# Kernel optimization log

Measured on AMD Instinct MI355X. Metric: run time of the kernel, lower is better.

Reference implementation:

```python
import jax, jax.numpy as jnp
import numpy as np

B, C, H, W = 2, 128, 192, 192
K = 9  # 3x3 kernel points
EPS = 1e-5


def conv3x3(x, w, b):
    # plain conv, stride 1, zero pad 1 (the pack's conv_offset_mask)
    out = jax.lax.conv_general_dilated(x, w, (1, 1), ((1, 1), (1, 1)),
                                       dimension_numbers=('NCHW', 'OIHW', 'NCHW'))
    return out + b[None, :, None, None]


def bilinear_gather(img, py, px):
    # img: (C,H,W); py/px: (K,H,W) float sampling coords; zero outside (DCNv2 semantics)
    y0 = jnp.floor(py)
    x0 = jnp.floor(px)
    ay = py - y0
    ax = px - x0
    y0i = y0.astype(jnp.int32)
    x0i = x0.astype(jnp.int32)

    def corner(yi, xi, wgt):
        valid = (yi >= 0) & (yi <= H - 1) & (xi >= 0) & (xi <= W - 1)
        yc = jnp.clip(yi, 0, H - 1)
        xc = jnp.clip(xi, 0, W - 1)
        v = img[:, yc, xc]  # (C,K,H,W) gather
        return v * (wgt * valid)[None]

    return (corner(y0i, x0i, (1 - ay) * (1 - ax))
            + corner(y0i, x0i + 1, (1 - ay) * ax)
            + corner(y0i + 1, x0i, ay * (1 - ax))
            + corner(y0i + 1, x0i + 1, ay * ax))


def dcn(x, lo, w_om, b_om, w, b):
    # ModulatedDeformConvPack: offsets+mask predicted from lo, deform conv applied to x
    om = conv3x3(lo, w_om, b_om)                      # (B, 3K, H, W)
    o1, o2, m = jnp.split(om, 3, axis=1)
    offset = jnp.concatenate([o1, o2], axis=1)        # (B, 2K, H, W)
    offset = offset.reshape(B, K, 2, H, W)            # channel 2k=y, 2k+1=x
    dy, dx = offset[:, :, 0], offset[:, :, 1]         # (B,K,H,W)
    mask = jax.nn.sigmoid(m)                          # (B,K,H,W)
    ky = jnp.array([-1, -1, -1, 0, 0, 0, 1, 1, 1], jnp.float32)
    kx = jnp.array([-1, 0, 1, -1, 0, 1, -1, 0, 1], jnp.float32)
    ii = jnp.arange(H, dtype=jnp.float32)[None, :, None]
    jj = jnp.arange(W, dtype=jnp.float32)[None, None, :]
    py = ii + ky[:, None, None] + dy                  # (B,K,H,W)
    px = jj + kx[:, None, None] + dx
    sampled = jax.vmap(bilinear_gather)(x, py, px)    # (B,C,K,H,W)
    sampled = sampled * mask[:, None]                 # modulation
    out = jnp.einsum('bckhw,ock->bohw', sampled, w.reshape(C, C, K))
    return out + b[None, :, None, None]


def inorm(x):
    # InstanceNorm2d(affine=False), eps=1e-5
    mu = x.mean((2, 3), keepdims=True)
    var = x.var((2, 3), keepdims=True)
    return (x - mu) * jax.lax.rsqrt(var + EPS)


def setup_inputs() -> dict:
    key = jax.random.key(0)
    ks = jax.random.split(key, 10)
    x = jax.random.normal(ks[0], (B, C, H, W), jnp.float32)
    lo = jax.random.normal(ks[1], (B, C, H, W), jnp.float32)
    # offset/mask conv kept small so sampling offsets stay near the grid
    w_om1 = jax.random.normal(ks[2], (3 * K, C, 3, 3), jnp.float32) * 0.01
    b_om1 = jnp.zeros((3 * K,), jnp.float32)
    w1 = jax.random.normal(ks[3], (C, C, 3, 3), jnp.float32) * 0.05
    b1 = jax.random.normal(ks[4], (C,), jnp.float32) * 0.02
    w_om2 = jax.random.normal(ks[5], (3 * K, C, 3, 3), jnp.float32) * 0.01
    b_om2 = jnp.zeros((3 * K,), jnp.float32)
    w2 = jax.random.normal(ks[6], (C, C, 3, 3), jnp.float32) * 0.05
    b2 = jax.random.normal(ks[7], (C,), jnp.float32) * 0.02
    return {'x': x, 'lo': lo, 'w_om1': w_om1, 'b_om1': b_om1, 'w1': w1, 'b1': b1,
            'w_om2': w_om2, 'b_om2': b_om2, 'w2': w2, 'b2': b2}


def reference(x, lo, w_om1, b_om1, w1, b1, w_om2, b_om2, w2, b2):
    r = jax.nn.relu(inorm(dcn(x, lo, w_om1, b_om1, w1, b1)))
    r = inorm(dcn(r, lo, w_om2, b_om2, w2, b2))
    return x + r
```

## Files before the change

### kernel.cpp

```cpp
#include <hip/hip_runtime.h>
#include <hip/hip_bf16.h>
#include <math.h>

#define BB 2
#define CCH 128
#define HH 192
#define WW 192
#define KK 9
#define HWs (HH*WW)
#define NPIX (BB*HWs)

typedef short bf16x8 __attribute__((ext_vector_type(8)));
typedef float f32x4 __attribute__((ext_vector_type(4)));

__device__ __forceinline__ int iclamp(int v, int lo, int hi) {
    return v < lo ? lo : (v > hi ? hi : v);
}
__device__ __forceinline__ unsigned short f2bf(float f) {
    union { __hip_bfloat16 h; unsigned short u; } cvt;
    cvt.h = __float2bfloat16(f);
    return cvt.u;
}
__device__ __forceinline__ float bflo(unsigned u) {
    return __uint_as_float(u << 16);
}
__device__ __forceinline__ float bfhi(unsigned u) {
    return __uint_as_float(u & 0xFFFF0000u);
}
__device__ __forceinline__ unsigned pkbf(float lo, float hi) {
    return (unsigned)f2bf(lo) | ((unsigned)f2bf(hi) << 16);
}

__global__ void transpose_wb_kernel(const float* __restrict__ in,
                                    unsigned short* __restrict__ outp) {
    int idx = blockIdx.x * 256 + threadIdx.x;
    if (idx >= 9 * CCH * CCH) return;
    int c = idx % CCH;
    int o = (idx / CCH) % CCH;
    int tap = idx / (CCH * CCH);
    outp[idx] = f2bf(in[(o * CCH + c) * 9 + tap]);
}

__global__ void transpose_womb_kernel(const float* __restrict__ in,
                                      unsigned short* __restrict__ outp) {
    int idx = blockIdx.x * 256 + threadIdx.x;
    if (idx >= 9 * 32 * CCH) return;
    int c = idx % CCH;
    int o = (idx / CCH) % 32;
    int tap = idx / (CCH * 32);
    outp[idx] = (o < 27) ? f2bf(in[(o * CCH + c) * 9 + tap]) : 0;
}

__global__ __launch_bounds__(256) void to_nhwc_bf16(
    const float* __restrict__ in, unsigned short* __restrict__ outp,
    const float* __restrict__ mu, const float* __restrict__ rs, int do_relu) {
    __shared__ float tile[CCH][33];
    int blk = blockIdx.x;
    int xt = blk % 6;
    int y = (blk / 6) % HH;
    int b = blk / (6 * HH);
    int x0 = xt * 32;
    int t = threadIdx.x;
    int xr = (t & 7) * 4;
    int cr = t >> 3;
#pragma unroll
    for (int it = 0; it < 4; ++it) {
        int c = it * 32 + cr;
        float4 v = *(const float4*)&in[((size_t)(b * CCH + c) * HH + y) * WW + x0 + xr];
        if (mu != nullptr) {
            float m = mu[b * CCH + c], r = rs[b * CCH + c];
            v.x = (v.x - m) * r; v.y = (v.y - m) * r;
            v.z = (v.z - m) * r; v.w = (v.w - m) * r;
        }
        if (do_relu) {
            v.x = fmaxf(v.x, 0.f); v.y = fmaxf(v.y, 0.f);
            v.z = fmaxf(v.z, 0.f); v.w = fmaxf(v.w, 0.f);
        }
        tile[c][xr] = v.x; tile[c][xr + 1] = v.y;
        tile[c][xr + 2] = v.z; tile[c][xr + 3] = v.w;
    }
    __syncthreads();
    int px = t >> 3;
    int wp = t & 7;
    size_t wbase = (((size_t)(b * HH + y)) * WW + x0 + px) * (CCH / 2);
    unsigned* outw = (unsigned*)outp;
#pragma unroll
    for (int it = 0; it < 8; ++it) {
        int ch = it * 16 + wp * 2;
        outw[wbase + it * 8 + wp] = pkbf(tile[ch][px], tile[ch + 1][px]);
    }
}

__global__ __launch_bounds__(256) void om_mfma_kernel(
    const unsigned short* __restrict__ lob,
    const unsigned short* __restrict__ Wob,
    const float* __restrict__ bom,
    float* __restrict__ samp) {
    __shared__ float s_om[4][16 * 33];
    int bid = blockIdx.x;
    int blk = (bid & 7) * 144 + (bid >> 3);
    int xt = blk % 3;
    int y = (blk / 3) % HH;
    int b = blk / (3 * HH);
    int t = threadIdx.x;
    int l = t & 63, q = l & 15, g = l >> 4, w = t >> 6;
    int px = xt * 64 + w * 16 + q;
    int cb = g * 8;
    f32x4 acc0 = (f32x4)0.f, acc1 = (f32x4)0.f;

    for (int k = 0; k < KK; ++k) {
        int ty = k / 3 - 1, tx = k % 3 - 1;
        int yy = y + ty, xx = px + tx;
        bool ok = (yy >= 0 && yy < HH && xx >= 0 && xx < WW);
        int yyc = iclamp(yy, 0, HH - 1), xxc = iclamp(xx, 0, WW - 1);
        const unsigned short* lrow = lob + ((size_t)(b * HH + yyc) * WW + xxc) * CCH;
#pragma unroll
        for (int ch = 0; ch < 4; ++ch) {
            bf16x8 a0 = *(const bf16x8*)&Wob[((size_t)k * 32 + q) * CCH + ch * 32 + cb];
            bf16x8 a1 = *(const bf16x8*)&Wob[((size_t)k * 32 + 16 + q) * CCH + ch * 32 + cb];
            bf16x8 bb = *(const bf16x8*)&lrow[ch * 32 + cb];
            if (!ok) bb = (bf16x8)0;
            acc0 = __builtin_amdgcn_mfma_f32_16x16x32_bf16(a0, bb, acc0, 0, 0, 0);
            acc1 = __builtin_amdgcn_mfma_f32_16x16x32_bf16(a1, bb, acc1, 0, 0, 0);
        }
    }
    float* so = s_om[w];
#pragma unroll
    for (int r = 0; r < 4; ++r) {
        int o0 = g * 4 + r;
        so[q * 33 + o0] = acc0[r] + bom[o0];
        int o1 = 16 + g * 4 + r;
        so[q * 33 + o1] = acc1[r] + ((o1 < 27) ? bom[o1] : 0.f);
    }
    __syncthreads();

    for (int tt = g; tt < 9; tt += 4) {
        float dy = so[q * 33 + 2 * tt];
        float dx = so[q * 33 + 2 * tt + 1];
        float ml = so[q * 33 + 18 + tt];
        float m = 1.0f / (1.0f + __expf(-ml));
        float py = (float)y + (float)(tt / 3 - 1) + dy;
        float pxf = (float)px + (float)(tt % 3 - 1) + dx;
        py = fminf(fmaxf(py, -2.0f), (float)(HH + 1));
        pxf = fminf(fmaxf(pxf, -2.0f), (float)(WW + 1));
        float y0f = floorf(py), x0f = floorf(pxf);
        float ay = py - y0f, ax = pxf - x0f;
        int y0 = (int)y0f, x0i = (int)x0f;
        int y1 = y0 + 1, x1 = x0i + 1;
        bool vy0 = (y0 >= 0 && y0 < HH), vy1 = (y1 >= 0 && y1 < HH);
        bool vx0 = (x0i >= 0 && x0i < WW), vx1 = (x1 >= 0 && x1 < WW);
        int y0c = iclamp(y0, 0, HH - 1), y1c = iclamp(y1, 0, HH - 1);
        int x0c = iclamp(x0i, 0, WW - 1), x1c = iclamp(x1, 0, WW - 1);
        float w00 = (1.0f - ay) * (1.0f - ax) * ((vy0 && vx0) ? m : 0.0f);
        float w01 = (1.0f - ay) * ax * ((vy0 && vx1) ? m : 0.0f);
        float w10 = ay * (1.0f - ax) * ((vy1 && vx0) ? m : 0.0f);
        float w11 = ay * ax * ((vy1 && vx1) ? m : 0.0f);
        float4 s0, s1;
        s0.x = __int_as_float(y0c * WW + x0c);
        s0.y = __int_as_float(y0c * WW + x1c);
        s0.z = __int_as_float(y1c * WW + x0c);
        s0.w = __int_as_float(y1c * WW + x1c);
        s1.x = w00; s1.y = w01; s1.z = w10; s1.w = w11;
        float* sp = samp + (((size_t)blk * 9 + tt) * 64 + w * 16 + q) * 8;
        *(float4*)sp = s0;
        *(float4*)(sp + 4) = s1;
    }
}

__global__ __launch_bounds__(256) void dcn_kernel(
    const unsigned short* __restrict__ xb,
    const float* __restrict__ samp,
    const unsigned short* __restrict__ Wb,
    const float* __restrict__ bias,
    float* __restrict__ outp) {
    __shared__ unsigned short s_w[CCH * CCH];
    int bid = blockIdx.x;
    int blk = (bid & 7) * 144 + (bid >> 3);
    int xt = blk % 3;
    int y = (blk / 3) % HH;
    int b = blk / (3 * HH);
    int t = threadIdx.x;
    int l = t & 63, q = l & 15, g = l >> 4, w = t >> 6;
    int px = xt * 64 + w * 16 + q;
    int cb = g * 8;
    int p_in = w * 16 + q;
    const unsigned short* xbb = xb + (size_t)b * HWs * CCH;
    const float* rec = samp + (size_t)blk * 9 * 64 * 8;
    char* swb = (char*)s_w;
    int swz_t = ((t >> 4) & 7) << 4;
    int xorq = (q & 7) << 4;

    f32x4 acc[8];
#pragma unroll
    for (int ot = 0; ot < 8; ++ot) acc[ot] = (f32x4)0.f;

    float4 rA = *(const float4*)(rec + (size_t)p_in * 8);
    float4 rB = *(const float4*)(rec + (size_t)p_in * 8 + 4);
    for (int k = 0; k < KK; ++k) {
        const char* wk = (const char*)(Wb + (size_t)k * CCH * CCH);
#pragma unroll
        for (int j = 0; j < 8; ++j) {
            int off = j * 4096 + t * 16;
            uint4 v = *(const uint4*)(wk + off);
            *(uint4*)(swb + (off ^ swz_t)) = v;
        }
        int kn = (k < 8) ? k + 1 : 8;
        float4 nA = *(const float4*)(rec + ((size_t)kn * 64 + p_in) * 8);
        float4 nB = *(const float4*)(rec + ((size_t)kn * 64 + p_in) * 8 + 4);
        int i00 = __float_as_int(rA.x);
        int i01 = __float_as_int(rA.y);
        int i10 = __float_as_int(rA.z);
        int i11 = __float_as_int(rA.w);
        const unsigned short* p00 = xbb + (size_t)i00 * CCH + cb;
        const unsigned short* p01 = xbb + (size_t)i01 * CCH + cb;
        const unsigned short* p10 = xbb + (size_t)i10 * CCH + cb;
        const unsigned short* p11 = xbb + (size_t)i11 * CCH + cb;
        bf16x8 bbv[4];
#pragma unroll
        for (int ch = 0; ch < 4; ++ch) {
            uint4 c00 = *(const uint4*)(p00 + ch * 32);
            uint4 c01 = *(const uint4*)(p01 + ch * 32);
            uint4 c10 = *(const uint4*)(p10 + ch * 32);
            uint4 c11 = *(const uint4*)(p11 + ch * 32);
            unsigned bbw[4];
            const unsigned* u00 = (const unsigned*)&c00;
            const unsigned* u01 = (const unsigned*)&c01;
            const unsigned* u10 = (const unsigned*)&c10;
            const unsigned* u11 = (const unsigned*)&c11;
#pragma unroll
            for (int d = 0; d < 4; ++d) {
                float slo = rB.x * bflo(u00[d]) + rB.y * bflo(u01[d]) +
                            rB.z * bflo(u10[d]) + rB.w * bflo(u11[d]);
                float shi = rB.x * bfhi(u00[d]) + rB.y * bfhi(u01[d]) +
                            rB.z * bfhi(u10[d]) + rB.w * bfhi(u11[d]);
                bbw[d] = pkbf(slo, shi);
            }
            uint4 bbu = make_uint4(bbw[0], bbw[1], bbw[2], bbw[3]);
            bbv[ch] = __builtin_bit_cast(bf16x8, bbu);
        }
        __syncthreads();
#pragma unroll
        for (int ch = 0; ch < 4; ++ch) {
            int inner = (ch * 64 + g * 16) ^ xorq;
#pragma unroll
            for (int ot = 0; ot < 8; ++ot) {
                bf16x8 a = *(const bf16x8*)(swb + (ot * 4096 + q * 256 + inner));
                acc[ot] = __builtin_amdgcn_mfma_f32_16x16x32_bf16(a, bbv[ch], acc[ot], 0, 0, 0);
            }
        }
        __syncthreads();
        rA = nA; rB = nB;
    }
#pragma unroll
    for (int ot = 0; ot < 8; ++ot) {
#pragma unroll
        for (int r = 0; r < 4; ++r) {
            int o = ot * 16 + g * 4 + r;
            outp[((size_t)(b * CCH + o) * HH + y) * WW + px] = acc[ot][r] + bias[o];
        }
    }
}

__global__ __launch_bounds__(256) void stats_kernel(
    const float* __restrict__ d, float* __restrict__ mu,
    float* __restrict__ rs) {
    int ch = blockIdx.x;
    const float* p = d + (size_t)ch * HWs;
    float s = 0.0f, s2 = 0.0f;
    for (int i = threadIdx.x; i < HWs / 4; i += 256) {
        float4 v = *(const float4*)&p[(size_t)i * 4];
        s += v.x + v.y + v.z + v.w;
        s2 += v.x * v.x + v.y * v.y + v.z * v.z + v.w * v.w;
    }
#pragma unroll
    for (int off = 32; off > 0; off >>= 1) {
        s += __shfl_down(s, off);
        s2 += __shfl_down(s2, off);
    }
    __shared__ float red[8];
    int wid = threadIdx.x >> 6;
    if ((threadIdx.x & 63) == 0) { red[wid] = s; red[4 + wid] = s2; }
    __syncthreads();
    if (threadIdx.x == 0) {
        s = red[0] + red[1] + red[2] + red[3];
        s2 = red[4] + red[5] + red[6] + red[7];
        float m = s / (float)HWs;
        float var = s2 / (float)HWs - m * m;
        mu[ch] = m;
        rs[ch] = rsqrtf(var + 1e-5f);
    }
}

__global__ __launch_bounds__(256) void final_kernel(
    const float* __restrict__ x, float* __restrict__ outp,
    const float* __restrict__ mu, const float* __restrict__ rs) {
    size_t i = ((size_t)blockIdx.x * 256 + threadIdx.x) * 4;
    int ch = (int)(i / HWs);
    float4 xv = *(const float4*)&x[i];
    float4 dv = *(const float4*)&outp[i];
    float m = mu[ch], r = rs[ch];
    float4 ov;
    ov.x = xv.x + (dv.x - m) * r;
    ov.y = xv.y + (dv.y - m) * r;
    ov.z = xv.z + (dv.z - m) * r;
    ov.w = xv.w + (dv.w - m) * r;
    *(float4*)&outp[i] = ov;
}

extern "C" void kernel_launch(void* const* d_in, const int* in_sizes, int n_in,
                              void* d_out, int out_size, void* d_ws,
                              size_t ws_size, hipStream_t stream) {
    (void)in_sizes; (void)n_in; (void)out_size; (void)ws_size;
    const float* x    = (const float*)d_in[0];
    const float* lo   = (const float*)d_in[1];
    const float* wom1 = (const float*)d_in[2];
    const float* bom1 = (const float*)d_in[3];
    const float* w1   = (const float*)d_in[4];
    const float* b1   = (const float*)d_in[5];
    const float* wom2 = (const float*)d_in[6];
    const float* bom2 = (const float*)d_in[7];
    const float* w2   = (const float*)d_in[8];
    const float* b2   = (const float*)d_in[9];
    float* out = (float*)d_out;

    char* wsb = (char*)d_ws;
    unsigned short* xbf  = (unsigned short*)wsb;
    unsigned short* lobf = (unsigned short*)(wsb + 18874368);
    float* samp = (float*)(wsb + 2 * 18874368);
    char* wp = wsb + 2 * 18874368 + 21233664;
    unsigned short* Wb1   = (unsigned short*)wp;
    unsigned short* Wb2   = (unsigned short*)(wp + 294912);
    unsigned short* Womb1 = (unsigned short*)(wp + 2 * 294912);
    unsigned short* Womb2 = (unsigned short*)(wp + 2 * 294912 + 73728);
    float* mu1 = (float*)(wp + 2 * 294912 + 2 * 73728);
    float* rs1 = mu1 + 256;
    float* mu2 = rs1 + 256;
    float* rs2 = mu2 + 256;

    transpose_wb_kernel<<<576, 256, 0, stream>>>(w1, Wb1);
    transpose_wb_kernel<<<576, 256, 0, stream>>>(w2, Wb2);
    transpose_womb_kernel<<<144, 256, 0, stream>>>(wom1, Womb1);
    transpose_womb_kernel<<<144, 256, 0, stream>>>(wom2, Womb2);

    to_nhwc_bf16<<<2304, 256, 0, stream>>>(x, xbf, nullptr, nullptr, 0);
    to_nhwc_bf16<<<2304, 256, 0, stream>>>(lo, lobf, nullptr, nullptr, 0);

    om_mfma_kernel<<<1152, 256, 0, stream>>>(lobf, Womb1, bom1, samp);
    dcn_kernel<<<1152, 256, 0, stream>>>(xbf, samp, Wb1, b1, out);
    stats_kernel<<<256, 256, 0, stream>>>(out, mu1, rs1);
    to_nhwc_bf16<<<2304, 256, 0, stream>>>(out, xbf, mu1, rs1, 1);

    om_mfma_kernel<<<1152, 256, 0, stream>>>(lobf, Womb2, bom2, samp);
    dcn_kernel<<<1152, 256, 0, stream>>>(xbf, samp, Wb2, b2, out);
    stats_kernel<<<256, 256, 0, stream>>>(out, mu2, rs2);

    final_kernel<<<9216, 256, 0, stream>>>(x, out, mu2, rs2);
}
```

Measured before the change: 450.9 us.

## Pre-gather all taps then double-buffer pre-swizzled weights in LDS

The DCN kernel now gathers and bilinearly interpolates the sampled inputs for all nine taps up front into registers (36 bf16x8 vectors per thread). It then runs the MFMA loop over a double-buffered LDS weight tile, prefetching the next tap's weights from global memory while the current tap computes, so there is one barrier per tap instead of two. The weight transpose kernel now writes the LDS swizzle into global memory, which removes the XOR from the staging stores. This raises register pressure considerably and doubles LDS use to 64KB per block, which could lower occupancy or cause spills.

```diff
diff --git a/kernel.cpp b/kernel.cpp
--- a/kernel.cpp
+++ b/kernel.cpp
@@ -31,14 +31,15 @@
     return (unsigned)f2bf(lo) | ((unsigned)f2bf(hi) << 16);
 }
 
-__global__ void transpose_wb_kernel(const float* __restrict__ in,
-                                    unsigned short* __restrict__ outp) {
+__global__ void transpose_wsw_kernel(const float* __restrict__ in,
+                                     unsigned short* __restrict__ outp) {
     int idx = blockIdx.x * 256 + threadIdx.x;
     if (idx >= 9 * CCH * CCH) return;
-    int c = idx % CCH;
-    int o = (idx / CCH) % CCH;
+    int col = idx % CCH;
+    int row = (idx / CCH) % CCH;
     int tap = idx / (CCH * CCH);
-    outp[idx] = f2bf(in[(o * CCH + c) * 9 + tap]);
+    int c = col ^ ((row & 7) << 3);
+    outp[idx] = f2bf(in[(row * CCH + c) * 9 + tap]);
 }
 
 __global__ void transpose_womb_kernel(const float* __restrict__ in,
@@ -170,10 +171,10 @@
 __global__ __launch_bounds__(256) void dcn_kernel(
     const unsigned short* __restrict__ xb,
     const float* __restrict__ samp,
-    const unsigned short* __restrict__ Wb,
+    const unsigned short* __restrict__ Wsw,
     const float* __restrict__ bias,
     float* __restrict__ outp) {
-    __shared__ unsigned short s_w[CCH * CCH];
+    __shared__ unsigned short s_w[2][CCH * CCH];
     int bid = blockIdx.x;
     int blk = (bid & 7) * 144 + (bid >> 3);
     int xt = blk % 3;
@@ -186,27 +187,13 @@
     int p_in = w * 16 + q;
     const unsigned short* xbb = xb + (size_t)b * HWs * CCH;
     const float* rec = samp + (size_t)blk * 9 * 64 * 8;
-    char* swb = (char*)s_w;
-    int swz_t = ((t >> 4) & 7) << 4;
     int xorq = (q & 7) << 4;
 
-    f32x4 acc[8];
-#pragma unroll
-    for (int ot = 0; ot < 8; ++ot) acc[ot] = (f32x4)0.f;
-
-    float4 rA = *(const float4*)(rec + (size_t)p_in * 8);
-    float4 rB = *(const float4*)(rec + (size_t)p_in * 8 + 4);
-    for (int k = 0; k < KK; ++k) {
-        const char* wk = (const char*)(Wb + (size_t)k * CCH * CCH);
-#pragma unroll
-        for (int j = 0; j < 8; ++j) {
-            int off = j * 4096 + t * 16;
-            uint4 v = *(const uint4*)(wk + off);
-            *(uint4*)(swb + (off ^ swz_t)) = v;
-        }
-        int kn = (k < 8) ? k + 1 : 8;
-        float4 nA = *(const float4*)(rec + ((size_t)kn * 64 + p_in) * 8);
-        float4 nB = *(const float4*)(rec + ((size_t)kn * 64 + p_in) * 8 + 4);
+    bf16x8 bbv[9][4];
+#pragma unroll
+    for (int k = 0; k < 9; ++k) {
+        float4 rA = *(const float4*)(rec + ((size_t)k * 64 + p_in) * 8);
+        float4 rB = *(const float4*)(rec + ((size_t)k * 64 + p_in) * 8 + 4);
         int i00 = __float_as_int(rA.x);
         int i01 = __float_as_int(rA.y);
         int i10 = __float_as_int(rA.z);
@@ -215,7 +202,6 @@
         const unsigned short* p01 = xbb + (size_t)i01 * CCH + cb;
         const unsigned short* p10 = xbb + (size_t)i10 * CCH + cb;
         const unsigned short* p11 = xbb + (size_t)i11 * CCH + cb;
-        bf16x8 bbv[4];
 #pragma unroll
         for (int ch = 0; ch < 4; ++ch) {
             uint4 c00 = *(const uint4*)(p00 + ch * 32);
@@ -236,21 +222,54 @@
                 bbw[d] = pkbf(slo, shi);
             }
             uint4 bbu = make_uint4(bbw[0], bbw[1], bbw[2], bbw[3]);
-            bbv[ch] = __builtin_bit_cast(bf16x8, bbu);
-        }
-        __syncthreads();
+            bbv[k][ch] = __builtin_bit_cast(bf16x8, bbu);
+        }
+    }
+
+    const char* wg = (const char*)Wsw;
+    {
+        uint4 st[8];
+#pragma unroll
+        for (int j = 0; j < 8; ++j)
+            st[j] = *(const uint4*)(wg + j * 4096 + t * 16);
+#pragma unroll
+        for (int j = 0; j < 8; ++j)
+            *(uint4*)((char*)s_w[0] + j * 4096 + t * 16) = st[j];
+    }
+    __syncthreads();
+
+    f32x4 acc[8];
+#pragma unroll
+    for (int ot = 0; ot < 8; ++ot) acc[ot] = (f32x4)0.f;
+
+#pragma unroll
+    for (int k = 0; k < 9; ++k) {
+        uint4 nx[8];
+        if (k < 8) {
+            const char* wn = wg + (size_t)(k + 1) * 32768;
+#pragma unroll
+            for (int j = 0; j < 8; ++j)
+                nx[j] = *(const uint4*)(wn + j * 4096 + t * 16);
+        }
+        char* swb = (char*)s_w[k & 1];
 #pragma unroll
         for (int ch = 0; ch < 4; ++ch) {
             int inner = (ch * 64 + g * 16) ^ xorq;
 #pragma unroll
             for (int ot = 0; ot < 8; ++ot) {
                 bf16x8 a = *(const bf16x8*)(swb + (ot * 4096 + q * 256 + inner));
-                acc[ot] = __builtin_amdgcn_mfma_f32_16x16x32_bf16(a, bbv[ch], acc[ot], 0, 0, 0);
+                acc[ot] = __builtin_amdgcn_mfma_f32_16x16x32_bf16(a, bbv[k][ch], acc[ot], 0, 0, 0);
             }
         }
+        if (k < 8) {
+            char* swn = (char*)s_w[(k + 1) & 1];
+#pragma unroll
+            for (int j = 0; j < 8; ++j)
+                *(uint4*)(swn + j * 4096 + t * 16) = nx[j];
+        }
         __syncthreads();
-        rA = nA; rB = nB;
-    }
+    }
+
 #pragma unroll
     for (int ot = 0; ot < 8; ++ot) {
 #pragma unroll
@@ -337,8 +356,8 @@
     float* mu2 = rs1 + 256;
     float* rs2 = mu2 + 256;
 
-    transpose_wb_kernel<<<576, 256, 0, stream>>>(w1, Wb1);
-    transpose_wb_kernel<<<576, 256, 0, stream>>>(w2, Wb2);
+    transpose_wsw_kernel<<<576, 256, 0, stream>>>(w1, Wb1);
+    transpose_wsw_kernel<<<576, 256, 0, stream>>>(w2, Wb2);
     transpose_womb_kernel<<<144, 256, 0, stream>>>(wom1, Womb1);
     transpose_womb_kernel<<<144, 256, 0, stream>>>(wom2, Womb2);
 
```

After: 535.5 us. 1.19x slower.
